# Performance work log

Hardware: AMD Instinct MI355X
Metric: run time of the kernel (lower is better)

## Reference

```python
import jax, jax.numpy as jnp
import numpy as np

N, E, D, K, NCONV = 50000, 800000, 64, 3, 6


def setup_inputs() -> dict:
    key = jax.random.key(0)
    ks = jax.random.split(key, 6)
    X = jax.random.normal(ks[0], (N, D), jnp.float32)
    edge_index = jax.random.randint(ks[1], (2, E), 0, N, dtype=jnp.int64)
    edge_weight = jax.random.uniform(ks[2], (E,), jnp.float32)
    H = jax.random.normal(ks[3], (N, D), jnp.float32)
    lambda_max = jnp.ones((1,), jnp.float32) * 2.0  # typical sym-normalized Laplacian bound
    conv_w = jax.random.normal(ks[4], (NCONV, K, D, D), jnp.float32) / np.sqrt(D)
    conv_b = jnp.zeros((NCONV, D), jnp.float32)
    return {"X": X, "edge_index": edge_index, "edge_weight": edge_weight,
            "H": H, "lambda_max": lambda_max, "conv_w": conv_w, "conv_b": conv_b}


def reference(X, edge_index, edge_weight, H, lambda_max, conv_w, conv_b):
    src, dst = edge_index[0], edge_index[1]
    # symmetric normalization: norm_e = w_e / sqrt(deg_src * deg_dst)
    deg = jax.ops.segment_sum(edge_weight, src, num_segments=N)
    dinv = jnp.where(deg > 0, deg ** -0.5, 0.0)
    norm = edge_weight * dinv[src] * dinv[dst]  # [E]
    lam = lambda_max.reshape(())
    c = 2.0 / lam

    def a_prop(v):  # A_norm @ v via scatter-add over edges, [N,D]
        return jax.ops.segment_sum(norm[:, None] * v[src], dst, num_segments=N)

    def l_hat(v):  # (2/lam)(I - A_norm) v - v
        return (c - 1.0) * v - c * a_prop(v)

    def cheb(v, w, b):  # ChebConv order K: sum_k T_k(L_hat) v @ W_k + b
        tx0, tx1 = v, l_hat(v)
        out = tx0 @ w[0] + tx1 @ w[1]
        for k in range(2, K):
            tx2 = 2.0 * l_hat(tx1) - tx0
            out = out + tx2 @ w[k]
            tx0, tx1 = tx1, tx2
        return out + b

    Z = jax.nn.sigmoid(cheb(X, conv_w[0], conv_b[0]) + cheb(H, conv_w[1], conv_b[1]))
    R = jax.nn.sigmoid(cheb(X, conv_w[2], conv_b[2]) + cheb(H, conv_w[3], conv_b[3]))
    H_tilde = jnp.tanh(cheb(X, conv_w[4], conv_b[4]) + cheb(H * R, conv_w[5], conv_b[5]))
    return Z * H_tilde + (1.0 - Z) * H
```

## Files before the change

### kernel.cpp

```cpp
#include <hip/hip_runtime.h>
#include <cstdint>
#include <cstddef>

typedef unsigned int u32;
typedef unsigned short u16;
typedef unsigned long long u64;

#define D 64
#define NCH 512
#define CAP 5120

typedef __attribute__((ext_vector_type(8))) short bf16x8;
typedef __attribute__((ext_vector_type(4))) float f32x4;

static __device__ __forceinline__ float sigmoidf_(float x) {
    return 1.f / (1.f + __expf(-x));
}
static __device__ __forceinline__ u16 f2bf(float x) {
    u32 u = __float_as_uint(x);
    return (u16)((u + 0x7fffu + ((u >> 16) & 1u)) >> 16);
}
static __device__ __forceinline__ u32 packbf2(float a, float b) {
    return (u32)f2bf(a) | ((u32)f2bf(b) << 16);
}
static __device__ __forceinline__ float bflo(u32 u) { return __uint_as_float(u << 16); }
static __device__ __forceinline__ float bfhi(u32 u) { return __uint_as_float(u & 0xffff0000u); }


__global__ void init_kernel(u32* cur_d, u32* cur_s) {
    int t = threadIdx.x;
    cur_d[t] = (u32)(t * CAP);
    cur_s[t] = (u32)(t * CAP);
}

__global__ __launch_bounds__(256) void coarse_kernel(
    const int* __restrict__ src, const int* __restrict__ dst, const float* __restrict__ w,
    u32* cur_d, u32* cur_s,
    u64* __restrict__ slab_d, u32* __restrict__ slab_s,
    int E, int CE) {
    __shared__ u32 hd[256], hs[256], cd[256], cs[256];
    int t = threadIdx.x, c = blockIdx.x;
    hd[t] = 0; hs[t] = 0;
    __syncthreads();
    int e0 = c * CE, e1 = min(E, e0 + CE);
    for (int e = e0 + t; e < e1; e += 256) {
        atomicAdd(&hd[(u32)dst[e] >> 8], 1u);
        atomicAdd(&hs[(u32)src[e] >> 8], 1u);
    }
    __syncthreads();
    cd[t] = atomicAdd(&cur_d[t], hd[t]);
    cs[t] = atomicAdd(&cur_s[t], hs[t]);
    __syncthreads();
    for (int e = e0 + t; e < e1; e += 256) {
        int s = src[e], d = dst[e];
        u32 wb = (u32)f2bf(w[e]);
        u32 pd = atomicAdd(&cd[(u32)d >> 8], 1u);
        u32 ps = atomicAdd(&cs[(u32)s >> 8], 1u);
        if (pd < (u32)(((d >> 8) + 1) * CAP))
            slab_d[pd] = (u64)((u32)s | (((u32)d & 255u) << 16)) | ((u64)wb << 32);
        if (ps < (u32)(((s >> 8) + 1) * CAP))
            slab_s[ps] = ((u32)s & 255u) | (wb << 16);
    }
}

__global__ void bprefix_kernel(const u32* __restrict__ cur_d, u32* __restrict__ bstart, int NB) {
    __shared__ int sd[256];
    int t = threadIdx.x;
    int v = (t < NB) ? min((int)cur_d[t] - t * CAP, CAP) : 0;
    sd[t] = v;
    __syncthreads();
    for (int o = 1; o < 256; o <<= 1) {
        int a = (t >= o) ? sd[t - o] : 0;
        __syncthreads();
        sd[t] += a;
        __syncthreads();
    }
    bstart[t] = (u32)(sd[t] - v);
}

__global__ __launch_bounds__(256) void fine_dst_kernel(
    const u64* __restrict__ slab, const u32* __restrict__ cur_d,
    const u32* __restrict__ bstart, u32* __restrict__ edge4,
    int* __restrict__ cnt, int* __restrict__ row_start, int N_) {
    __shared__ int h[256], sd[256], cur[256];
    int b = blockIdx.x, t = threadIdx.x;
    int m = min((int)cur_d[b] - b * CAP, CAP);
    const u64* rp = slab + (size_t)b * CAP;
    h[t] = 0;
    __syncthreads();
    for (int i = t; i < m; i += 256) atomicAdd(&h[(int)((rp[i] >> 16) & 255u)], 1);
    __syncthreads();
    int v = h[t];
    sd[t] = v;
    __syncthreads();
    for (int o = 1; o < 256; o <<= 1) {
        int a = (t >= o) ? sd[t - o] : 0;
        __syncthreads();
        sd[t] += a;
        __syncthreads();
    }
    int excl = sd[t] - v;
    cur[t] = excl;
    int bs = (int)bstart[b];
    int node = (b << 8) + t;
    if (node < N_) { cnt[node] = v; row_start[node] = bs + excl; }
    __syncthreads();
    for (int i = t; i < m; i += 256) {
        u64 r = rp[i];
        int f = (int)((r >> 16) & 255u);
        int p = atomicAdd(&cur[f], 1);
        edge4[bs + p] = (u32)(r & 0xffffu) | ((u32)(r >> 32) << 16);
    }
}

__global__ __launch_bounds__(256) void fine_deg_kernel(
    const u32* __restrict__ slab_s, const u32* __restrict__ cur_s,
    float* __restrict__ dinv, int N_) {
    __shared__ float dg[256];
    int b = blockIdx.x, t = threadIdx.x;
    int m = min((int)cur_s[b] - b * CAP, CAP);
    const u32* rp = slab_s + (size_t)b * CAP;
    dg[t] = 0.f;
    __syncthreads();
    for (int i = t; i < m; i += 256) {
        u32 r = rp[i];
        atomicAdd(&dg[r & 255u], __uint_as_float(r & 0xffff0000u));
    }
    __syncthreads();
    int node = (b << 8) + t;
    if (node < N_) dinv[node] = (dg[t] > 0.f) ? rsqrtf(dg[t]) : 0.f;
}


__global__ void xh2_kernel(const float* __restrict__ X, const float* __restrict__ H,
                           const float* __restrict__ dinv,
                           u32* __restrict__ XH_u, u32* __restrict__ XH_t, int total) {
    int i = blockIdx.x * blockDim.x + threadIdx.x;
    if (i >= total) return;
    int nn = i >> 6, l = i & 63;
    const float* sp = (l < 32 ? X : H) + (size_t)nn * 64 + ((2 * l) & 63);
    float2 v = *(const float2*)sp;
    float dv = dinv[nn];
    XH_t[i] = packbf2(v.x, v.y);
    XH_u[i] = packbf2(v.x * dv, v.y * dv);
}

__global__ __launch_bounds__(256) void wt_kernel(const float* __restrict__ w, u32* __restrict__ WT) {
    __shared__ float s[64][68];
    int g = blockIdx.x, t = threadIdx.x;
    const float* wp = w + (size_t)g * 4096;
    for (int i = t; i < 1024; i += 256) {
        int k = i >> 4, c4 = (i & 15) * 4;
        *(float4*)&s[k][c4] = *(const float4*)&wp[k * 64 + c4];
    }
    __syncthreads();
    for (int i = t; i < 2048; i += 256) {
        int uk = i & 31, n = i >> 5;
        WT[(size_t)g * 2048 + n * 32 + uk] = packbf2(s[2 * uk][n], s[2 * uk + 1][n]);
    }
}


__global__ __launch_bounds__(256) void lhat128_kernel(
    const u32* __restrict__ vu, const u32* __restrict__ vt, const u32* __restrict__ w0t,
    u32* __restrict__ out_t, u32* __restrict__ out_u,
    const int* __restrict__ rs, const int* __restrict__ cnt, const float* __restrict__ dinv,
    const u32* __restrict__ edges, const float* __restrict__ lam_ptr, int n) {
    int node = (blockIdx.x * blockDim.x + threadIdx.x) >> 6;
    if (node >= n) return;
    int l = threadIdx.x & 63;
    int g = l >> 4, f = l & 15;
    int e0 = rs[node], end = e0 + cnt[node];
    float acc[8];
#pragma unroll
    for (int j = 0; j < 8; j++) acc[j] = 0.f;

    int base = e0;
    for (; base + 16 <= end; base += 16) {
        u32 r0 = edges[base + g];
        u32 r1 = edges[base + 4 + g];
        u32 r2 = edges[base + 8 + g];
        u32 r3 = edges[base + 12 + g];
        const uint4 q0 = *(const uint4*)(vu + (size_t)(r0 & 0xffffu) * 64 + 4 * f);
        const uint4 q1 = *(const uint4*)(vu + (size_t)(r1 & 0xffffu) * 64 + 4 * f);
        const uint4 q2 = *(const uint4*)(vu + (size_t)(r2 & 0xffffu) * 64 + 4 * f);
        const uint4 q3 = *(const uint4*)(vu + (size_t)(r3 & 0xffffu) * 64 + 4 * f);
        float n0 = __uint_as_float(r0 & 0xffff0000u);
        float n1 = __uint_as_float(r1 & 0xffff0000u);
        float n2 = __uint_as_float(r2 & 0xffff0000u);
        float n3 = __uint_as_float(r3 & 0xffff0000u);
        acc[0] += n0 * bflo(q0.x); acc[1] += n0 * bfhi(q0.x);
        acc[2] += n0 * bflo(q0.y); acc[3] += n0 * bfhi(q0.y);
        acc[4] += n0 * bflo(q0.z); acc[5] += n0 * bfhi(q0.z);
        acc[6] += n0 * bflo(q0.w); acc[7] += n0 * bfhi(q0.w);
        acc[0] += n1 * bflo(q1.x); acc[1] += n1 * bfhi(q1.x);
        acc[2] += n1 * bflo(q1.y); acc[3] += n1 * bfhi(q1.y);
        acc[4] += n1 * bflo(q1.z); acc[5] += n1 * bfhi(q1.z);
        acc[6] += n1 * bflo(q1.w); acc[7] += n1 * bfhi(q1.w);
        acc[0] += n2 * bflo(q2.x); acc[1] += n2 * bfhi(q2.x);
        acc[2] += n2 * bflo(q2.y); acc[3] += n2 * bfhi(q2.y);
        acc[4] += n2 * bflo(q2.z); acc[5] += n2 * bfhi(q2.z);
        acc[6] += n2 * bflo(q2.w); acc[7] += n2 * bfhi(q2.w);
        acc[0] += n3 * bflo(q3.x); acc[1] += n3 * bfhi(q3.x);
        acc[2] += n3 * bflo(q3.y); acc[3] += n3 * bfhi(q3.y);
        acc[4] += n3 * bflo(q3.z); acc[5] += n3 * bfhi(q3.z);
        acc[6] += n3 * bflo(q3.w); acc[7] += n3 * bfhi(q3.w);
    }
    for (; base < end; base += 4) {
        int ei = base + g;
        u32 r0 = (ei < end) ? edges[ei] : 0u;
        const uint4 q0 = *(const uint4*)(vu + (size_t)(r0 & 0xffffu) * 64 + 4 * f);
        float n0 = __uint_as_float(r0 & 0xffff0000u);
        acc[0] += n0 * bflo(q0.x); acc[1] += n0 * bfhi(q0.x);
        acc[2] += n0 * bflo(q0.y); acc[3] += n0 * bfhi(q0.y);
        acc[4] += n0 * bflo(q0.z); acc[5] += n0 * bfhi(q0.z);
        acc[6] += n0 * bflo(q0.w); acc[7] += n0 * bfhi(q0.w);
    }
#pragma unroll
    for (int m = 16; m <= 32; m <<= 1)
#pragma unroll
        for (int j = 0; j < 8; j++) acc[j] += __shfl_xor(acc[j], m);

    const uint4 sv = *(const uint4*)(vt + (size_t)node * 64 + 4 * f);
    float self[8];
    self[0] = bflo(sv.x); self[1] = bfhi(sv.x);
    self[2] = bflo(sv.y); self[3] = bfhi(sv.y);
    self[4] = bflo(sv.z); self[5] = bfhi(sv.z);
    self[6] = bflo(sv.w); self[7] = bfhi(sv.w);
    float c = 2.f / lam_ptr[0];
    float dv = dinv[node];
    float rx[8];
#pragma unroll
    for (int j = 0; j < 8; j++) rx[j] = (c - 1.f) * self[j] - (c * dv) * acc[j];
    if (w0t) {
        const uint4 wv4 = *(const uint4*)(w0t + (size_t)node * 64 + 4 * f);
        rx[0] = 2.f * rx[0] - bflo(wv4.x); rx[1] = 2.f * rx[1] - bfhi(wv4.x);
        rx[2] = 2.f * rx[2] - bflo(wv4.y); rx[3] = 2.f * rx[3] - bfhi(wv4.y);
        rx[4] = 2.f * rx[4] - bflo(wv4.z); rx[5] = 2.f * rx[5] - bfhi(wv4.z);
        rx[6] = 2.f * rx[6] - bflo(wv4.w); rx[7] = 2.f * rx[7] - bfhi(wv4.w);
    }
    if (l < 16) {
        uint4 o;
        o.x = packbf2(rx[0], rx[1]); o.y = packbf2(rx[2], rx[3]);
        o.z = packbf2(rx[4], rx[5]); o.w = packbf2(rx[6], rx[7]);
        *(uint4*)(out_t + (size_t)node * 64 + 4 * f) = o;
        if (out_u) {
            uint4 ou;
            ou.x = packbf2(rx[0] * dv, rx[1] * dv); ou.y = packbf2(rx[2] * dv, rx[3] * dv);
            ou.z = packbf2(rx[4] * dv, rx[5] * dv); ou.w = packbf2(rx[6] * dv, rx[7] * dv);
            *(uint4*)(out_u + (size_t)node * 64 + 4 * f) = ou;
        }
    }
}

__global__ __launch_bounds__(256) void lhat64_kernel(
    const u32* __restrict__ vu, const u32* __restrict__ vt, const u32* __restrict__ w0t,
    u32* __restrict__ out_t, u32* __restrict__ out_u,
    const int* __restrict__ rs, const int* __restrict__ cnt, const float* __restrict__ dinv,
    const u32* __restrict__ edges, const float* __restrict__ lam_ptr, int n) {
    int node = (blockIdx.x * blockDim.x + threadIdx.x) >> 6;
    if (node >= n) return;
    int l = threadIdx.x & 63;
    int g = l >> 3, f = l & 7;
    int e0 = rs[node], end = e0 + cnt[node];
    float acc[8];
#pragma unroll
    for (int j = 0; j < 8; j++) acc[j] = 0.f;

    int base = e0;
    for (; base + 16 <= end; base += 16) {
        u32 r0 = edges[base + g];
        u32 r1 = edges[base + 8 + g];
        const uint4 q0 = *(const uint4*)(vu + (size_t)(r0 & 0xffffu) * 32 + 4 * f);
        const uint4 q1 = *(const uint4*)(vu + (size_t)(r1 & 0xffffu) * 32 + 4 * f);
        float n0 = __uint_as_float(r0 & 0xffff0000u);
        float n1 = __uint_as_float(r1 & 0xffff0000u);
        acc[0] += n0 * bflo(q0.x); acc[1] += n0 * bfhi(q0.x);
        acc[2] += n0 * bflo(q0.y); acc[3] += n0 * bfhi(q0.y);
        acc[4] += n0 * bflo(q0.z); acc[5] += n0 * bfhi(q0.z);
        acc[6] += n0 * bflo(q0.w); acc[7] += n0 * bfhi(q0.w);
        acc[0] += n1 * bflo(q1.x); acc[1] += n1 * bfhi(q1.x);
        acc[2] += n1 * bflo(q1.y); acc[3] += n1 * bfhi(q1.y);
        acc[4] += n1 * bflo(q1.z); acc[5] += n1 * bfhi(q1.z);
        acc[6] += n1 * bflo(q1.w); acc[7] += n1 * bfhi(q1.w);
    }
    for (; base < end; base += 8) {
        int ei = base + g;
        u32 r0 = (ei < end) ? edges[ei] : 0u;
        const uint4 q0 = *(const uint4*)(vu + (size_t)(r0 & 0xffffu) * 32 + 4 * f);
        float n0 = __uint_as_float(r0 & 0xffff0000u);
        acc[0] += n0 * bflo(q0.x); acc[1] += n0 * bfhi(q0.x);
        acc[2] += n0 * bflo(q0.y); acc[3] += n0 * bfhi(q0.y);
        acc[4] += n0 * bflo(q0.z); acc[5] += n0 * bfhi(q0.z);
        acc[6] += n0 * bflo(q0.w); acc[7] += n0 * bfhi(q0.w);
    }
#pragma unroll
    for (int m = 8; m <= 32; m <<= 1)
#pragma unroll
        for (int j = 0; j < 8; j++) acc[j] += __shfl_xor(acc[j], m);

    const uint4 sv = *(const uint4*)(vt + (size_t)node * 32 + 4 * f);
    float self[8];
    self[0] = bflo(sv.x); self[1] = bfhi(sv.x);
    self[2] = bflo(sv.y); self[3] = bfhi(sv.y);
    self[4] = bflo(sv.z); self[5] = bfhi(sv.z);
    self[6] = bflo(sv.w); self[7] = bfhi(sv.w);
    float c = 2.f / lam_ptr[0];
    float dv = dinv[node];
    float rx[8];
#pragma unroll
    for (int j = 0; j < 8; j++) rx[j] = (c - 1.f) * self[j] - (c * dv) * acc[j];
    if (w0t) {
        const uint4 wv4 = *(const uint4*)(w0t + (size_t)node * 32 + 4 * f);
        rx[0] = 2.f * rx[0] - bflo(wv4.x); rx[1] = 2.f * rx[1] - bfhi(wv4.x);
        rx[2] = 2.f * rx[2] - bflo(wv4.y); rx[3] = 2.f * rx[3] - bfhi(wv4.y);
        rx[4] = 2.f * rx[4] - bflo(wv4.z); rx[5] = 2.f * rx[5] - bfhi(wv4.z);
        rx[6] = 2.f * rx[6] - bflo(wv4.w); rx[7] = 2.f * rx[7] - bfhi(wv4.w);
    }
    if (l < 8) {
        uint4 o;
        o.x = packbf2(rx[0], rx[1]); o.y = packbf2(rx[2], rx[3]);
        o.z = packbf2(rx[4], rx[5]); o.w = packbf2(rx[6], rx[7]);
        *(uint4*)(out_t + (size_t)node * 32 + 4 * f) = o;
        if (out_u) {
            uint4 ou;
            ou.x = packbf2(rx[0] * dv, rx[1] * dv); ou.y = packbf2(rx[2] * dv, rx[3] * dv);
            ou.z = packbf2(rx[4] * dv, rx[5] * dv); ou.w = packbf2(rx[6] * dv, rx[7] * dv);
            *(uint4*)(out_u + (size_t)node * 32 + 4 * f) = ou;
        }
    }
}

__global__ __launch_bounds__(256) void gemm_gate_kernel(
    const u32* __restrict__ A0, const u32* __restrict__ A1, const u32* __restrict__ A2,
    const u32* __restrict__ WT, const float* __restrict__ convb,
    const float* __restrict__ Hf, const float* __restrict__ dinv,
    float* __restrict__ Zb, float* __restrict__ Sh,
    u16* __restrict__ HR_t, u16* __restrict__ HR_u, int n) {
    __shared__ u32 Ws[64 * 36];
    int t = threadIdx.x;
    int wv = t >> 6, l = t & 63;
    int q = l >> 4, ml = l & 15;
    int R = blockIdx.x * 64 + wv * 16;
    int ar = R + ml; if (ar >= n) ar = n - 1;

    f32x4 S[3][4];
#pragma unroll
    for (int tg = 0; tg < 3; tg++)
#pragma unroll
        for (int ni = 0; ni < 4; ni++) S[tg][ni] = (f32x4){0.f, 0.f, 0.f, 0.f};

    for (int kt = 0; kt < 3; kt++) {
        const u32* Ap = (kt == 0) ? A0 : ((kt == 1) ? A1 : A2);
        const u32* ap = Ap + (size_t)ar * 64 + q * 4;
        bf16x8 af[2][2];
        af[0][0] = *(const bf16x8*)(ap +  0);
        af[1][0] = *(const bf16x8*)(ap + 16);
        af[0][1] = *(const bf16x8*)(ap + 32);
        af[1][1] = *(const bf16x8*)(ap + 48);
#pragma unroll
        for (int cg = 0; cg < 5; cg++) {
            int hf = cg & 1, tg = cg >> 1;
            const u32* Wp = WT + (size_t)(cg * 3 + kt) * 2048;
            __syncthreads();
            {
                int i0 = t * 4, i1 = i0 + 1024;
                uint4 w0 = *(const uint4*)(Wp + i0);
                uint4 w1 = *(const uint4*)(Wp + i1);
                *(uint4*)&Ws[(i0 >> 5) * 36 + (i0 & 31)] = w0;
                *(uint4*)&Ws[(i1 >> 5) * 36 + (i1 & 31)] = w1;
            }
            __syncthreads();
#pragma unroll
            for (int h = 0; h < 2; h++) {
                bf16x8 bw[4];
#pragma unroll
                for (int ni = 0; ni < 4; ni++)
                    bw[ni] = *(const bf16x8*)&Ws[(ni * 16 + ml) * 36 + q * 4 + h * 16];
#pragma unroll
                for (int ni = 0; ni < 4; ni++)
                    S[tg][ni] = __builtin_amdgcn_mfma_f32_16x16x32_bf16(
                        af[h][hf], bw[ni], S[tg][ni], 0, 0, 0);
            }
        }
    }
#pragma unroll
    for (int ni = 0; ni < 4; ni++) {
        int col = ni * 16 + ml;
        float bz = convb[col] + convb[64 + col];
        float br = convb[128 + col] + convb[192 + col];
#pragma unroll
        for (int reg = 0; reg < 4; reg++) {
            int row = R + q * 4 + reg;
            if (row < n) {
                size_t o = (size_t)row * 64 + col;
                float z = sigmoidf_(S[0][ni][reg] + bz);
                float r = sigmoidf_(S[1][ni][reg] + br);
                float hr = Hf[o] * r;
                float dv = dinv[row];
                Zb[o] = z;
                Sh[o] = S[2][ni][reg];
                HR_t[o] = f2bf(hr);
                HR_u[o] = f2bf(hr * dv);
            }
        }
    }
}

__global__ __launch_bounds__(256) void gemm_final_kernel(
    const u32* __restrict__ A0, const u32* __restrict__ A1, const u32* __restrict__ A2,
    const u32* __restrict__ WT, const float* __restrict__ convb,
    const float* __restrict__ Zb, const float* __restrict__ Sh, const float* __restrict__ Hf,
    float* __restrict__ outp, int n) {
    __shared__ u32 Ws[64 * 36];
    int t = threadIdx.x;
    int wv = t >> 6, l = t & 63;
    int q = l >> 4, ml = l & 15;
    int R = blockIdx.x * 64 + wv * 16;
    int ar = R + ml; if (ar >= n) ar = n - 1;

    f32x4 S[4];
#pragma unroll
    for (int ni = 0; ni < 4; ni++) S[ni] = (f32x4){0.f, 0.f, 0.f, 0.f};

    for (int kt = 0; kt < 3; kt++) {
        const u32* Ap = (kt == 0) ? A0 : ((kt == 1) ? A1 : A2);
        const u32* ap = Ap + (size_t)ar * 32 + q * 4;
        bf16x8 af[2];
        af[0] = *(const bf16x8*)(ap +  0);
        af[1] = *(const bf16x8*)(ap + 16);
        const u32* Wp = WT + (size_t)(15 + kt) * 2048;
        __syncthreads();
        {
            int i0 = t * 4, i1 = i0 + 1024;
            uint4 w0 = *(const uint4*)(Wp + i0);
            uint4 w1 = *(const uint4*)(Wp + i1);
            *(uint4*)&Ws[(i0 >> 5) * 36 + (i0 & 31)] = w0;
            *(uint4*)&Ws[(i1 >> 5) * 36 + (i1 & 31)] = w1;
        }
        __syncthreads();
#pragma unroll
        for (int h = 0; h < 2; h++) {
            bf16x8 bw[4];
#pragma unroll
            for (int ni = 0; ni < 4; ni++)
                bw[ni] = *(const bf16x8*)&Ws[(ni * 16 + ml) * 36 + q * 4 + h * 16];
#pragma unroll
            for (int ni = 0; ni < 4; ni++)
                S[ni] = __builtin_amdgcn_mfma_f32_16x16x32_bf16(af[h], bw[ni], S[ni], 0, 0, 0);
        }
    }
#pragma unroll
    for (int ni = 0; ni < 4; ni++) {
        int col = ni * 16 + ml;
        float bh = convb[256 + col] + convb[320 + col];
#pragma unroll
        for (int reg = 0; reg < 4; reg++) {
            int row = R + q * 4 + reg;
            if (row < n) {
                size_t o = (size_t)row * 64 + col;
                float z = Zb[o];
                float ht = tanhf(S[ni][reg] + Sh[o] + bh);
                outp[o] = z * ht + (1.f - z) * Hf[o];
            }
        }
    }
}


extern "C" void kernel_launch(void* const* d_in, const int* in_sizes, int n_in,
                              void* d_out, int out_size, void* d_ws, size_t ws_size,
                              hipStream_t stream) {
    const float* X     = (const float*)d_in[0];
    const int*   ei    = (const int*)d_in[1];
    const float* ew    = (const float*)d_in[2];
    const float* H     = (const float*)d_in[3];
    const float* lam   = (const float*)d_in[4];
    const float* convw = (const float*)d_in[5];
    const float* convb = (const float*)d_in[6];
    float* out = (float*)d_out;

    const int N = in_sizes[0] / D;
    const int E = in_sizes[2];
    const int* src = ei;
    const int* dst = ei + E;

    const int NB = (N + 255) >> 8;
    const int CE = (E + NCH - 1) / NCH;

    char* p = (char*)d_ws;
    auto alloc = [&](size_t bytes) {
        void* r = (void*)p;
        p += (bytes + 255) & ~(size_t)255;
        return r;
    };
    float* Zb   = (float*)alloc((size_t)N * 64 * 4);
    float* Sh   = (float*)alloc((size_t)N * 64 * 4);
    u32* XH_u = (u32*)alloc((size_t)N * 64 * 4);
    u32* XH_t = (u32*)alloc((size_t)N * 64 * 4);
    u32* T1_u = (u32*)alloc((size_t)N * 64 * 4);
    u32* T1_t = (u32*)alloc((size_t)N * 64 * 4);
    u32* T2_t = (u32*)alloc((size_t)N * 64 * 4);
    u16* HR_u = (u16*)alloc((size_t)N * 64 * 2);
    u16* HR_t = (u16*)alloc((size_t)N * 64 * 2);
    u16* U1_u = (u16*)alloc((size_t)N * 64 * 2);
    u16* U1_t = (u16*)alloc((size_t)N * 64 * 2);
    u16* U2_t = (u16*)alloc((size_t)N * 64 * 2);
    u32* edge4 = (u32*)alloc((size_t)E * 4);
    u64* slab_d = (u64*)alloc((size_t)NB * CAP * 8);
    u32* slab_s = (u32*)alloc((size_t)NB * CAP * 4);
    u32* cur_d  = (u32*)alloc(256 * 4);
    u32* cur_s  = (u32*)alloc(256 * 4);
    u32* bstart = (u32*)alloc(256 * 4);
    int* cnt       = (int*)alloc((size_t)N * 4);
    int* row_start = (int*)alloc((size_t)N * 4);
    float* dinv    = (float*)alloc((size_t)N * 4);
    u32* WT = (u32*)alloc((size_t)18 * 2048 * 4);

    const int BLK = 256;
    const int gND  = (N * D + BLK - 1) / BLK;
    const int gWav = gND;
    const int gx64 = (N + 63) / 64;

    init_kernel<<<1, 256, 0, stream>>>(cur_d, cur_s);
    coarse_kernel<<<NCH, BLK, 0, stream>>>(src, dst, ew, cur_d, cur_s, slab_d, slab_s, E, CE);
    bprefix_kernel<<<1, 256, 0, stream>>>(cur_d, bstart, NB);
    fine_dst_kernel<<<NB, BLK, 0, stream>>>(slab_d, cur_d, bstart, edge4, cnt, row_start, N);
    fine_deg_kernel<<<NB, BLK, 0, stream>>>(slab_s, cur_s, dinv, N);

    wt_kernel<<<18, BLK, 0, stream>>>(convw, WT);
    xh2_kernel<<<gND, BLK, 0, stream>>>(X, H, dinv, XH_u, XH_t, N * D);

    lhat128_kernel<<<gWav, BLK, 0, stream>>>(XH_u, XH_t, nullptr, T1_t, T1_u,
                                             row_start, cnt, dinv, edge4, lam, N);
    lhat128_kernel<<<gWav, BLK, 0, stream>>>(T1_u, T1_t, XH_t, T2_t, nullptr,
                                             row_start, cnt, dinv, edge4, lam, N);

    gemm_gate_kernel<<<gx64, BLK, 0, stream>>>(XH_t, T1_t, T2_t, WT, convb, H, dinv,
                                               Zb, Sh, HR_t, HR_u, N);

    lhat64_kernel<<<gWav, BLK, 0, stream>>>((const u32*)HR_u, (const u32*)HR_t, nullptr,
                                            (u32*)U1_t, (u32*)U1_u,
                                            row_start, cnt, dinv, edge4, lam, N);
    lhat64_kernel<<<gWav, BLK, 0, stream>>>((const u32*)U1_u, (const u32*)U1_t, (const u32*)HR_t,
                                            (u32*)U2_t, nullptr,
                                            row_start, cnt, dinv, edge4, lam, N);

    gemm_final_kernel<<<gx64, BLK, 0, stream>>>((const u32*)HR_t, (const u32*)U1_t, (const u32*)U2_t,
                                                WT, convb, Zb, Sh, H, out, N);
}
```

Baseline: 302.9 us.

## Compute degree with global atomics and grid-stride lhat kernels over nodes

Removes the source-side slab binning and the separate degree kernel; edge weights are atomically added into a zeroed global degree array, and dinv is computed inside xh2. The lhat propagation kernels now use a fixed 2048-block grid that loops over nodes, instead of launching one wave per element index where most blocks exit immediately. This saves slab writes, one kernel launch and idle block scheduling, at the cost of global float atomic contention and nondeterministic summation order.

New measurement: 352.0 us. +16.2%, slower.

```diff
diff --git a/kernel.cpp b/kernel.cpp
--- a/kernel.cpp
+++ b/kernel.cpp
@@ -27,39 +27,36 @@
 static __device__ __forceinline__ float bfhi(u32 u) { return __uint_as_float(u & 0xffff0000u); }
 
 
-__global__ void init_kernel(u32* cur_d, u32* cur_s) {
-    int t = threadIdx.x;
-    cur_d[t] = (u32)(t * CAP);
-    cur_s[t] = (u32)(t * CAP);
+__global__ void init_kernel(u32* cur_d, float* deg, int N_) {
+    int i = blockIdx.x * blockDim.x + threadIdx.x;
+    if (i < N_) deg[i] = 0.f;
+    if (blockIdx.x == 0) cur_d[threadIdx.x] = (u32)(threadIdx.x * CAP);
 }
 
 __global__ __launch_bounds__(256) void coarse_kernel(
     const int* __restrict__ src, const int* __restrict__ dst, const float* __restrict__ w,
-    u32* cur_d, u32* cur_s,
-    u64* __restrict__ slab_d, u32* __restrict__ slab_s,
+    u32* cur_d, float* __restrict__ deg,
+    u64* __restrict__ slab_d,
     int E, int CE) {
-    __shared__ u32 hd[256], hs[256], cd[256], cs[256];
+    __shared__ u32 hd[256], cd[256];
     int t = threadIdx.x, c = blockIdx.x;
-    hd[t] = 0; hs[t] = 0;
+    hd[t] = 0;
     __syncthreads();
     int e0 = c * CE, e1 = min(E, e0 + CE);
     for (int e = e0 + t; e < e1; e += 256) {
         atomicAdd(&hd[(u32)dst[e] >> 8], 1u);
-        atomicAdd(&hs[(u32)src[e] >> 8], 1u);
     }
     __syncthreads();
     cd[t] = atomicAdd(&cur_d[t], hd[t]);
-    cs[t] = atomicAdd(&cur_s[t], hs[t]);
     __syncthreads();
     for (int e = e0 + t; e < e1; e += 256) {
         int s = src[e], d = dst[e];
-        u32 wb = (u32)f2bf(w[e]);
+        float wf = w[e];
+        atomicAdd(&deg[s], wf);
+        u32 wb = (u32)f2bf(wf);
         u32 pd = atomicAdd(&cd[(u32)d >> 8], 1u);
-        u32 ps = atomicAdd(&cs[(u32)s >> 8], 1u);
         if (pd < (u32)(((d >> 8) + 1) * CAP))
             slab_d[pd] = (u64)((u32)s | (((u32)d & 255u) << 16)) | ((u64)wb << 32);
-        if (ps < (u32)(((s >> 8) + 1) * CAP))
-            slab_s[ps] = ((u32)s & 255u) | (wb << 16);
     }
 }
 
@@ -113,34 +110,18 @@
     }
 }
 
-__global__ __launch_bounds__(256) void fine_deg_kernel(
-    const u32* __restrict__ slab_s, const u32* __restrict__ cur_s,
-    float* __restrict__ dinv, int N_) {
-    __shared__ float dg[256];
-    int b = blockIdx.x, t = threadIdx.x;
-    int m = min((int)cur_s[b] - b * CAP, CAP);
-    const u32* rp = slab_s + (size_t)b * CAP;
-    dg[t] = 0.f;
-    __syncthreads();
-    for (int i = t; i < m; i += 256) {
-        u32 r = rp[i];
-        atomicAdd(&dg[r & 255u], __uint_as_float(r & 0xffff0000u));
-    }
-    __syncthreads();
-    int node = (b << 8) + t;
-    if (node < N_) dinv[node] = (dg[t] > 0.f) ? rsqrtf(dg[t]) : 0.f;
-}
-
 
 __global__ void xh2_kernel(const float* __restrict__ X, const float* __restrict__ H,
-                           const float* __restrict__ dinv,
+                           const float* __restrict__ deg, float* __restrict__ dinv,
                            u32* __restrict__ XH_u, u32* __restrict__ XH_t, int total) {
     int i = blockIdx.x * blockDim.x + threadIdx.x;
     if (i >= total) return;
     int nn = i >> 6, l = i & 63;
+    float dg = deg[nn];
+    float dv = (dg > 0.f) ? rsqrtf(dg) : 0.f;
+    if (l == 0) dinv[nn] = dv;
     const float* sp = (l < 32 ? X : H) + (size_t)nn * 64 + ((2 * l) & 63);
     float2 v = *(const float2*)sp;
-    float dv = dinv[nn];
     XH_t[i] = packbf2(v.x, v.y);
     XH_u[i] = packbf2(v.x * dv, v.y * dv);
 }
@@ -166,89 +147,92 @@
     u32* __restrict__ out_t, u32* __restrict__ out_u,
     const int* __restrict__ rs, const int* __restrict__ cnt, const float* __restrict__ dinv,
     const u32* __restrict__ edges, const float* __restrict__ lam_ptr, int n) {
-    int node = (blockIdx.x * blockDim.x + threadIdx.x) >> 6;
-    if (node >= n) return;
+    int wid0 = (blockIdx.x * blockDim.x + threadIdx.x) >> 6;
+    int nwv = (gridDim.x * blockDim.x) >> 6;
     int l = threadIdx.x & 63;
     int g = l >> 4, f = l & 15;
-    int e0 = rs[node], end = e0 + cnt[node];
-    float acc[8];
-#pragma unroll
-    for (int j = 0; j < 8; j++) acc[j] = 0.f;
-
-    int base = e0;
-    for (; base + 16 <= end; base += 16) {
-        u32 r0 = edges[base + g];
-        u32 r1 = edges[base + 4 + g];
-        u32 r2 = edges[base + 8 + g];
-        u32 r3 = edges[base + 12 + g];
-        const uint4 q0 = *(const uint4*)(vu + (size_t)(r0 & 0xffffu) * 64 + 4 * f);
-        const uint4 q1 = *(const uint4*)(vu + (size_t)(r1 & 0xffffu) * 64 + 4 * f);
-        const uint4 q2 = *(const uint4*)(vu + (size_t)(r2 & 0xffffu) * 64 + 4 * f);
-        const uint4 q3 = *(const uint4*)(vu + (size_t)(r3 & 0xffffu) * 64 + 4 * f);
-        float n0 = __uint_as_float(r0 & 0xffff0000u);
-        float n1 = __uint_as_float(r1 & 0xffff0000u);
-        float n2 = __uint_as_float(r2 & 0xffff0000u);
-        float n3 = __uint_as_float(r3 & 0xffff0000u);
-        acc[0] += n0 * bflo(q0.x); acc[1] += n0 * bfhi(q0.x);
-        acc[2] += n0 * bflo(q0.y); acc[3] += n0 * bfhi(q0.y);
-        acc[4] += n0 * bflo(q0.z); acc[5] += n0 * bfhi(q0.z);
-        acc[6] += n0 * bflo(q0.w); acc[7] += n0 * bfhi(q0.w);
-        acc[0] += n1 * bflo(q1.x); acc[1] += n1 * bfhi(q1.x);
-        acc[2] += n1 * bflo(q1.y); acc[3] += n1 * bfhi(q1.y);
-        acc[4] += n1 * bflo(q1.z); acc[5] += n1 * bfhi(q1.z);
-        acc[6] += n1 * bflo(q1.w); acc[7] += n1 * bfhi(q1.w);
-        acc[0] += n2 * bflo(q2.x); acc[1] += n2 * bfhi(q2.x);
-        acc[2] += n2 * bflo(q2.y); acc[3] += n2 * bfhi(q2.y);
-        acc[4] += n2 * bflo(q2.z); acc[5] += n2 * bfhi(q2.z);
-        acc[6] += n2 * bflo(q2.w); acc[7] += n2 * bfhi(q2.w);
-        acc[0] += n3 * bflo(q3.x); acc[1] += n3 * bfhi(q3.x);
-        acc[2] += n3 * bflo(q3.y); acc[3] += n3 * bfhi(q3.y);
-        acc[4] += n3 * bflo(q3.z); acc[5] += n3 * bfhi(q3.z);
-        acc[6] += n3 * bflo(q3.w); acc[7] += n3 * bfhi(q3.w);
-    }
-    for (; base < end; base += 4) {
-        int ei = base + g;
-        u32 r0 = (ei < end) ? edges[ei] : 0u;
-        const uint4 q0 = *(const uint4*)(vu + (size_t)(r0 & 0xffffu) * 64 + 4 * f);
-        float n0 = __uint_as_float(r0 & 0xffff0000u);
-        acc[0] += n0 * bflo(q0.x); acc[1] += n0 * bfhi(q0.x);
-        acc[2] += n0 * bflo(q0.y); acc[3] += n0 * bfhi(q0.y);
-        acc[4] += n0 * bflo(q0.z); acc[5] += n0 * bfhi(q0.z);
-        acc[6] += n0 * bflo(q0.w); acc[7] += n0 * bfhi(q0.w);
-    }
-#pragma unroll
-    for (int m = 16; m <= 32; m <<= 1)
-#pragma unroll
-        for (int j = 0; j < 8; j++) acc[j] += __shfl_xor(acc[j], m);
-
-    const uint4 sv = *(const uint4*)(vt + (size_t)node * 64 + 4 * f);
-    float self[8];
-    self[0] = bflo(sv.x); self[1] = bfhi(sv.x);
-    self[2] = bflo(sv.y); self[3] = bfhi(sv.y);
-    self[4] = bflo(sv.z); self[5] = bfhi(sv.z);
-    self[6] = bflo(sv.w); self[7] = bfhi(sv.w);
     float c = 2.f / lam_ptr[0];
-    float dv = dinv[node];
-    float rx[8];
-#pragma unroll
-    for (int j = 0; j < 8; j++) rx[j] = (c - 1.f) * self[j] - (c * dv) * acc[j];
-    if (w0t) {
-        const uint4 wv4 = *(const uint4*)(w0t + (size_t)node * 64 + 4 * f);
-        rx[0] = 2.f * rx[0] - bflo(wv4.x); rx[1] = 2.f * rx[1] - bfhi(wv4.x);
-        rx[2] = 2.f * rx[2] - bflo(wv4.y); rx[3] = 2.f * rx[3] - bfhi(wv4.y);
-        rx[4] = 2.f * rx[4] - bflo(wv4.z); rx[5] = 2.f * rx[5] - bfhi(wv4.z);
-        rx[6] = 2.f * rx[6] - bflo(wv4.w); rx[7] = 2.f * rx[7] - bfhi(wv4.w);
-    }
-    if (l < 16) {
-        uint4 o;
-        o.x = packbf2(rx[0], rx[1]); o.y = packbf2(rx[2], rx[3]);
-        o.z = packbf2(rx[4], rx[5]); o.w = packbf2(rx[6], rx[7]);
-        *(uint4*)(out_t + (size_t)node * 64 + 4 * f) = o;
-        if (out_u) {
-            uint4 ou;
-            ou.x = packbf2(rx[0] * dv, rx[1] * dv); ou.y = packbf2(rx[2] * dv, rx[3] * dv);
-            ou.z = packbf2(rx[4] * dv, rx[5] * dv); ou.w = packbf2(rx[6] * dv, rx[7] * dv);
-            *(uint4*)(out_u + (size_t)node * 64 + 4 * f) = ou;
+
+    for (int node = wid0; node < n; node += nwv) {
+        int e0 = rs[node], end = e0 + cnt[node];
+        float acc[8];
+#pragma unroll
+        for (int j = 0; j < 8; j++) acc[j] = 0.f;
+
+        int base = e0;
+        for (; base + 16 <= end; base += 16) {
+            u32 r0 = edges[base + g];
+            u32 r1 = edges[base + 4 + g];
+            u32 r2 = edges[base + 8 + g];
+            u32 r3 = edges[base + 12 + g];
+            const uint4 q0 = *(const uint4*)(vu + (size_t)(r0 & 0xffffu) * 64 + 4 * f);
+            const uint4 q1 = *(const uint4*)(vu + (size_t)(r1 & 0xffffu) * 64 + 4 * f);
+            const uint4 q2 = *(const uint4*)(vu + (size_t)(r2 & 0xffffu) * 64 + 4 * f);
+            const uint4 q3 = *(const uint4*)(vu + (size_t)(r3 & 0xffffu) * 64 + 4 * f);
+            float n0 = __uint_as_float(r0 & 0xffff0000u);
+            float n1 = __uint_as_float(r1 & 0xffff0000u);
+            float n2 = __uint_as_float(r2 & 0xffff0000u);
+            float n3 = __uint_as_float(r3 & 0xffff0000u);
+            acc[0] += n0 * bflo(q0.x); acc[1] += n0 * bfhi(q0.x);
+            acc[2] += n0 * bflo(q0.y); acc[3] += n0 * bfhi(q0.y);
+            acc[4] += n0 * bflo(q0.z); acc[5] += n0 * bfhi(q0.z);
+            acc[6] += n0 * bflo(q0.w); acc[7] += n0 * bfhi(q0.w);
+            acc[0] += n1 * bflo(q1.x); acc[1] += n1 * bfhi(q1.x);
+            acc[2] += n1 * bflo(q1.y); acc[3] += n1 * bfhi(q1.y);
+            acc[4] += n1 * bflo(q1.z); acc[5] += n1 * bfhi(q1.z);
+            acc[6] += n1 * bflo(q1.w); acc[7] += n1 * bfhi(q1.w);
+            acc[0] += n2 * bflo(q2.x); acc[1] += n2 * bfhi(q2.x);
+            acc[2] += n2 * bflo(q2.y); acc[3] += n2 * bfhi(q2.y);
+            acc[4] += n2 * bflo(q2.z); acc[5] += n2 * bfhi(q2.z);
+            acc[6] += n2 * bflo(q2.w); acc[7] += n2 * bfhi(q2.w);
+            acc[0] += n3 * bflo(q3.x); acc[1] += n3 * bfhi(q3.x);
+            acc[2] += n3 * bflo(q3.y); acc[3] += n3 * bfhi(q3.y);
+            acc[4] += n3 * bflo(q3.z); acc[5] += n3 * bfhi(q3.z);
+            acc[6] += n3 * bflo(q3.w); acc[7] += n3 * bfhi(q3.w);
+        }
+        for (; base < end; base += 4) {
+            int ei = base + g;
+            u32 r0 = (ei < end) ? edges[ei] : 0u;
+            const uint4 q0 = *(const uint4*)(vu + (size_t)(r0 & 0xffffu) * 64 + 4 * f);
+            float n0 = __uint_as_float(r0 & 0xffff0000u);
+            acc[0] += n0 * bflo(q0.x); acc[1] += n0 * bfhi(q0.x);
+            acc[2] += n0 * bflo(q0.y); acc[3] += n0 * bfhi(q0.y);
+            acc[4] += n0 * bflo(q0.z); acc[5] += n0 * bfhi(q0.z);
+            acc[6] += n0 * bflo(q0.w); acc[7] += n0 * bfhi(q0.w);
+        }
+#pragma unroll
+        for (int m = 16; m <= 32; m <<= 1)
+#pragma unroll
+            for (int j = 0; j < 8; j++) acc[j] += __shfl_xor(acc[j], m);
+
+        const uint4 sv = *(const uint4*)(vt + (size_t)node * 64 + 4 * f);
+        float self[8];
+        self[0] = bflo(sv.x); self[1] = bfhi(sv.x);
+        self[2] = bflo(sv.y); self[3] = bfhi(sv.y);
+        self[4] = bflo(sv.z); self[5] = bfhi(sv.z);
+        self[6] = bflo(sv.w); self[7] = bfhi(sv.w);
+        float dv = dinv[node];
+        float rx[8];
+#pragma unroll
+        for (int j = 0; j < 8; j++) rx[j] = (c - 1.f) * self[j] - (c * dv) * acc[j];
+        if (w0t) {
+            const uint4 wv4 = *(const uint4*)(w0t + (size_t)node * 64 + 4 * f);
+            rx[0] = 2.f * rx[0] - bflo(wv4.x); rx[1] = 2.f * rx[1] - bfhi(wv4.x);
+            rx[2] = 2.f * rx[2] - bflo(wv4.y); rx[3] = 2.f * rx[3] - bfhi(wv4.y);
+            rx[4] = 2.f * rx[4] - bflo(wv4.z); rx[5] = 2.f * rx[5] - bfhi(wv4.z);
+            rx[6] = 2.f * rx[6] - bflo(wv4.w); rx[7] = 2.f * rx[7] - bfhi(wv4.w);
+        }
+        if (l < 16) {
+            uint4 o;
+            o.x = packbf2(rx[0], rx[1]); o.y = packbf2(rx[2], rx[3]);
+            o.z = packbf2(rx[4], rx[5]); o.w = packbf2(rx[6], rx[7]);
+            *(uint4*)(out_t + (size_t)node * 64 + 4 * f) = o;
+            if (out_u) {
+                uint4 ou;
+                ou.x = packbf2(rx[0] * dv, rx[1] * dv); ou.y = packbf2(rx[2] * dv, rx[3] * dv);
+                ou.z = packbf2(rx[4] * dv, rx[5] * dv); ou.w = packbf2(rx[6] * dv, rx[7] * dv);
+                *(uint4*)(out_u + (size_t)node * 64 + 4 * f) = ou;
+            }
         }
     }
 }
@@ -258,75 +242,78 @@
     u32* __restrict__ out_t, u32* __restrict__ out_u,
     const int* __restrict__ rs, const int* __restrict__ cnt, const float* __restrict__ dinv,
     const u32* __restrict__ edges, const float* __restrict__ lam_ptr, int n) {
-    int node = (blockIdx.x * blockDim.x + threadIdx.x) >> 6;
-    if (node >= n) return;
+    int wid0 = (blockIdx.x * blockDim.x + threadIdx.x) >> 6;
+    int nwv = (gridDim.x * blockDim.x) >> 6;
     int l = threadIdx.x & 63;
     int g = l >> 3, f = l & 7;
-    int e0 = rs[node], end = e0 + cnt[node];
-    float acc[8];
-#pragma unroll
-    for (int j = 0; j < 8; j++) acc[j] = 0.f;
-
-    int base = e0;
-    for (; base + 16 <= end; base += 16) {
-        u32 r0 = edges[base + g];
-        u32 r1 = edges[base + 8 + g];
-        const uint4 q0 = *(const uint4*)(vu + (size_t)(r0 & 0xffffu) * 32 + 4 * f);
-        const uint4 q1 = *(const uint4*)(vu + (size_t)(r1 & 0xffffu) * 32 + 4 * f);
-        float n0 = __uint_as_float(r0 & 0xffff0000u);
-        float n1 = __uint_as_float(r1 & 0xffff0000u);
-        acc[0] += n0 * bflo(q0.x); acc[1] += n0 * bfhi(q0.x);
-        acc[2] += n0 * bflo(q0.y); acc[3] += n0 * bfhi(q0.y);
-        acc[4] += n0 * bflo(q0.z); acc[5] += n0 * bfhi(q0.z);
-        acc[6] += n0 * bflo(q0.w); acc[7] += n0 * bfhi(q0.w);
-        acc[0] += n1 * bflo(q1.x); acc[1] += n1 * bfhi(q1.x);
-        acc[2] += n1 * bflo(q1.y); acc[3] += n1 * bfhi(q1.y);
-        acc[4] += n1 * bflo(q1.z); acc[5] += n1 * bfhi(q1.z);
-        acc[6] += n1 * bflo(q1.w); acc[7] += n1 * bfhi(q1.w);
-    }
-    for (; base < end; base += 8) {
-        int ei = base + g;
-        u32 r0 = (ei < end) ? edges[ei] : 0u;
-        const uint4 q0 = *(const uint4*)(vu + (size_t)(r0 & 0xffffu) * 32 + 4 * f);
-        float n0 = __uint_as_float(r0 & 0xffff0000u);
-        acc[0] += n0 * bflo(q0.x); acc[1] += n0 * bfhi(q0.x);
-        acc[2] += n0 * bflo(q0.y); acc[3] += n0 * bfhi(q0.y);
-        acc[4] += n0 * bflo(q0.z); acc[5] += n0 * bfhi(q0.z);
-        acc[6] += n0 * bflo(q0.w); acc[7] += n0 * bfhi(q0.w);
-    }
-#pragma unroll
-    for (int m = 8; m <= 32; m <<= 1)
-#pragma unroll
-        for (int j = 0; j < 8; j++) acc[j] += __shfl_xor(acc[j], m);
-
-    const uint4 sv = *(const uint4*)(vt + (size_t)node * 32 + 4 * f);
-    float self[8];
-    self[0] = bflo(sv.x); self[1] = bfhi(sv.x);
-    self[2] = bflo(sv.y); self[3] = bfhi(sv.y);
-    self[4] = bflo(sv.z); self[5] = bfhi(sv.z);
-    self[6] = bflo(sv.w); self[7] = bfhi(sv.w);
     float c = 2.f / lam_ptr[0];
-    float dv = dinv[node];
-    float rx[8];
-#pragma unroll
-    for (int j = 0; j < 8; j++) rx[j] = (c - 1.f) * self[j] - (c * dv) * acc[j];
-    if (w0t) {
-        const uint4 wv4 = *(const uint4*)(w0t + (size_t)node * 32 + 4 * f);
-        rx[0] = 2.f * rx[0] - bflo(wv4.x); rx[1] = 2.f * rx[1] - bfhi(wv4.x);
-        rx[2] = 2.f * rx[2] - bflo(wv4.y); rx[3] = 2.f * rx[3] - bfhi(wv4.y);
-        rx[4] = 2.f * rx[4] - bflo(wv4.z); rx[5] = 2.f * rx[5] - bfhi(wv4.z);
-        rx[6] = 2.f * rx[6] - bflo(wv4.w); rx[7] = 2.f * rx[7] - bfhi(wv4.w);
-    }
-    if (l < 8) {
-        uint4 o;
-        o.x = packbf2(rx[0], rx[1]); o.y = packbf2(rx[2], rx[3]);
-        o.z = packbf2(rx[4], rx[5]); o.w = packbf2(rx[6], rx[7]);
-        *(uint4*)(out_t + (size_t)node * 32 + 4 * f) = o;
-        if (out_u) {
-            uint4 ou;
-            ou.x = packbf2(rx[0] * dv, rx[1] * dv); ou.y = packbf2(rx[2] * dv, rx[3] * dv);
-            ou.z = packbf2(rx[4] * dv, rx[5] * dv); ou.w = packbf2(rx[6] * dv, rx[7] * dv);
-            *(uint4*)(out_u + (size_t)node * 32 + 4 * f) = ou;
+
+    for (int node = wid0; node < n; node += nwv) {
+        int e0 = rs[node], end = e0 + cnt[node];
+        float acc[8];
+#pragma unroll
+        for (int j = 0; j < 8; j++) acc[j] = 0.f;
+
+        int base = e0;
+        for (; base + 16 <= end; base += 16) {
+            u32 r0 = edges[base + g];
+            u32 r1 = edges[base + 8 + g];
+            const uint4 q0 = *(const uint4*)(vu + (size_t)(r0 & 0xffffu) * 32 + 4 * f);
+            const uint4 q1 = *(const uint4*)(vu + (size_t)(r1 & 0xffffu) * 32 + 4 * f);
+            float n0 = __uint_as_float(r0 & 0xffff0000u);
+            float n1 = __uint_as_float(r1 & 0xffff0000u);
+            acc[0] += n0 * bflo(q0.x); acc[1] += n0 * bfhi(q0.x);
+            acc[2] += n0 * bflo(q0.y); acc[3] += n0 * bfhi(q0.y);
+            acc[4] += n0 * bflo(q0.z); acc[5] += n0 * bfhi(q0.z);
+            acc[6] += n0 * bflo(q0.w); acc[7] += n0 * bfhi(q0.w);
+            acc[0] += n1 * bflo(q1.x); acc[1] += n1 * bfhi(q1.x);
+            acc[2] += n1 * bflo(q1.y); acc[3] += n1 * bfhi(q1.y);
+            acc[4] += n1 * bflo(q1.z); acc[5] += n1 * bfhi(q1.z);
+            acc[6] += n1 * bflo(q1.w); acc[7] += n1 * bfhi(q1.w);
+        }
+        for (; base < end; base += 8) {
+            int ei = base + g;
+            u32 r0 = (ei < end) ? edges[ei] : 0u;
+            const uint4 q0 = *(const uint4*)(vu + (size_t)(r0 & 0xffffu) * 32 + 4 * f);
+            float n0 = __uint_as_float(r0 & 0xffff0000u);
+            acc[0] += n0 * bflo(q0.x); acc[1] += n0 * bfhi(q0.x);
+            acc[2] += n0 * bflo(q0.y); acc[3] += n0 * bfhi(q0.y);
+            acc[4] += n0 * bflo(q0.z); acc[5] += n0 * bfhi(q0.z);
+            acc[6] += n0 * bflo(q0.w); acc[7] += n0 * bfhi(q0.w);
+        }
+#pragma unroll
+        for (int m = 8; m <= 32; m <<= 1)
+#pragma unroll
+            for (int j = 0; j < 8; j++) acc[j] += __shfl_xor(acc[j], m);
+
+        const uint4 sv = *(const uint4*)(vt + (size_t)node * 32 + 4 * f);
+        float self[8];
+        self[0] = bflo(sv.x); self[1] = bfhi(sv.x);
+        self[2] = bflo(sv.y); self[3] = bfhi(sv.y);
+        self[4] = bflo(sv.z); self[5] = bfhi(sv.z);
+        self[6] = bflo(sv.w); self[7] = bfhi(sv.w);
+        float dv = dinv[node];
+        float rx[8];
+#pragma unroll
+        for (int j = 0; j < 8; j++) rx[j] = (c - 1.f) * self[j] - (c * dv) * acc[j];
+        if (w0t) {
+            const uint4 wv4 = *(const uint4*)(w0t + (size_t)node * 32 + 4 * f);
+            rx[0] = 2.f * rx[0] - bflo(wv4.x); rx[1] = 2.f * rx[1] - bfhi(wv4.x);
+            rx[2] = 2.f * rx[2] - bflo(wv4.y); rx[3] = 2.f * rx[3] - bfhi(wv4.y);
+            rx[4] = 2.f * rx[4] - bflo(wv4.z); rx[5] = 2.f * rx[5] - bfhi(wv4.z);
+            rx[6] = 2.f * rx[6] - bflo(wv4.w); rx[7] = 2.f * rx[7] - bfhi(wv4.w);
+        }
+        if (l < 8) {
+            uint4 o;
+            o.x = packbf2(rx[0], rx[1]); o.y = packbf2(rx[2], rx[3]);
+            o.z = packbf2(rx[4], rx[5]); o.w = packbf2(rx[6], rx[7]);
+            *(uint4*)(out_t + (size_t)node * 32 + 4 * f) = o;
+            if (out_u) {
+                uint4 ou;
+                ou.x = packbf2(rx[0] * dv, rx[1] * dv); ou.y = packbf2(rx[2] * dv, rx[3] * dv);
+                ou.z = packbf2(rx[4] * dv, rx[5] * dv); ou.w = packbf2(rx[6] * dv, rx[7] * dv);
+                *(uint4*)(out_u + (size_t)node * 32 + 4 * f) = ou;
+            }
         }
     }
 }
@@ -508,43 +495,42 @@
     u16* U2_t = (u16*)alloc((size_t)N * 64 * 2);
     u32* edge4 = (u32*)alloc((size_t)E * 4);
     u64* slab_d = (u64*)alloc((size_t)NB * CAP * 8);
-    u32* slab_s = (u32*)alloc((size_t)NB * CAP * 4);
     u32* cur_d  = (u32*)alloc(256 * 4);
-    u32* cur_s  = (u32*)alloc(256 * 4);
     u32* bstart = (u32*)alloc(256 * 4);
     int* cnt       = (int*)alloc((size_t)N * 4);
     int* row_start = (int*)alloc((size_t)N * 4);
+    float* deg     = (float*)alloc((size_t)N * 4);
     float* dinv    = (float*)alloc((size_t)N * 4);
     u32* WT = (u32*)alloc((size_t)18 * 2048 * 4);
 
     const int BLK = 256;
     const int gND  = (N * D + BLK - 1) / BLK;
-    const int gWav = gND;
+    const int gNZ  = (N + BLK - 1) / BLK;
     const int gx64 = (N + 63) / 64;
-
-    init_kernel<<<1, 256, 0, stream>>>(cur_d, cur_s);
-    coarse_kernel<<<NCH, BLK, 0, stream>>>(src, dst, ew, cur_d, cur_s, slab_d, slab_s, E, CE);
+    const int gLH  = 2048;
+
+    init_kernel<<<gNZ, BLK, 0, stream>>>(cur_d, deg, N);
+    coarse_kernel<<<NCH, BLK, 0, stream>>>(src, dst, ew, cur_d, deg, slab_d, E, CE);
     bprefix_kernel<<<1, 256, 0, stream>>>(cur_d, bstart, NB);
     fine_dst_kernel<<<NB, BLK, 0, stream>>>(slab_d, cur_d, bstart, edge4, cnt, row_start, N);
-    fine_deg_kernel<<<NB, BLK, 0, stream>>>(slab_s, cur_s, dinv, N);
 
     wt_kernel<<<18, BLK, 0, stream>>>(convw, WT);
-    xh2_kernel<<<gND, BLK, 0, stream>>>(X, H, dinv, XH_u, XH_t, N * D);
-
-    lhat128_kernel<<<gWav, BLK, 0, stream>>>(XH_u, XH_t, nullptr, T1_t, T1_u,
-                                             row_start, cnt, dinv, edge4, lam, N);
-    lhat128_kernel<<<gWav, BLK, 0, stream>>>(T1_u, T1_t, XH_t, T2_t, nullptr,
-                                             row_start, cnt, dinv, edge4, lam, N);
+    xh2_kernel<<<gND, BLK, 0, stream>>>(X, H, deg, dinv, XH_u, XH_t, N * D);
+
+    lhat128_kernel<<<gLH, BLK, 0, stream>>>(XH_u, XH_t, nullptr, T1_t, T1_u,
+                                            row_start, cnt, dinv, edge4, lam, N);
+    lhat128_kernel<<<gLH, BLK, 0, stream>>>(T1_u, T1_t, XH_t, T2_t, nullptr,
+                                            row_start, cnt, dinv, edge4, lam, N);
 
     gemm_gate_kernel<<<gx64, BLK, 0, stream>>>(XH_t, T1_t, T2_t, WT, convb, H, dinv,
                                                Zb, Sh, HR_t, HR_u, N);
 
-    lhat64_kernel<<<gWav, BLK, 0, stream>>>((const u32*)HR_u, (const u32*)HR_t, nullptr,
-                                            (u32*)U1_t, (u32*)U1_u,
-                                            row_start, cnt, dinv, edge4, lam, N);
-    lhat64_kernel<<<gWav, BLK, 0, stream>>>((const u32*)U1_u, (const u32*)U1_t, (const u32*)HR_t,
-                                            (u32*)U2_t, nullptr,
-                                            row_start, cnt, dinv, edge4, lam, N);
+    lhat64_kernel<<<gLH, BLK, 0, stream>>>((const u32*)HR_u, (const u32*)HR_t, nullptr,
+                                           (u32*)U1_t, (u32*)U1_u,
+                                           row_start, cnt, dinv, edge4, lam, N);
+    lhat64_kernel<<<gLH, BLK, 0, stream>>>((const u32*)U1_u, (const u32*)U1_t, (const u32*)HR_t,
+                                           (u32*)U2_t, nullptr,
+                                           row_start, cnt, dinv, edge4, lam, N);
 
     gemm_final_kernel<<<gx64, BLK, 0, stream>>>((const u32*)HR_t, (const u32*)U1_t, (const u32*)U2_t,
                                                 WT, convb, Zb, Sh, H, out, N);
```
